# Optimization experiments

Hardware: AMD Instinct MI355X
Metric: run time of the kernel (lower is better)

Reference implementation:

```python
import jax, jax.numpy as jnp
import numpy as np

B, C, H, W = 16, 256, 96, 96


def setup_inputs() -> dict:
    key = jax.random.key(0)
    ks = jax.random.split(key, 10)
    s = 1.0 / np.sqrt(C)
    return {
        "x": jax.random.normal(ks[0], (B, C, H, W), dtype=jnp.float32) * 0.1,
        "w_theta": jax.random.normal(ks[1], (C, C), dtype=jnp.float32) * s,
        "b_theta": jax.random.normal(ks[2], (C,), dtype=jnp.float32) * 0.01,
        "w_phi": jax.random.normal(ks[3], (C, C), dtype=jnp.float32) * s,
        "b_phi": jax.random.normal(ks[4], (C,), dtype=jnp.float32) * 0.01,
        "w_g": jax.random.normal(ks[5], (C, C), dtype=jnp.float32) * s,
        "b_g": jax.random.normal(ks[6], (C,), dtype=jnp.float32) * 0.01,
        "beta_w": jax.random.normal(ks[7], (), dtype=jnp.float32) * 0.1,
        "beta_h": jax.random.normal(ks[8], (), dtype=jnp.float32) * 0.1,
        "beta_c": jax.random.normal(ks[9], (), dtype=jnp.float32) * 0.1,
    }


def _conv1x1(x, w, b):
    # 1x1 conv == channel mixing: [B,C,H,W] x [O,C] -> [B,O,H,W]
    return jnp.einsum('bchw,oc->bohw', x, w) + b[None, :, None, None]


def _axis_att(q, k, v, perm):
    # perm maps [B,C,H,W] -> [B, axis, rest...]; attention over `axis`
    qp = jnp.transpose(q, perm)
    kp = jnp.transpose(k, perm)
    vp = jnp.transpose(v, perm)
    shp = vp.shape
    n = shp[1]
    qf = qp.reshape(shp[0], n, -1)
    kf = kp.reshape(shp[0], n, -1)
    vf = vp.reshape(shp[0], n, -1)
    att = jax.nn.softmax(jnp.einsum('bik,bjk->bij', qf, kf), axis=-1)  # [B,n,n]
    out = jnp.einsum('bij,bjk->bik', att, vf).reshape(shp)
    inv = np.argsort(perm)
    return jnp.transpose(out, inv)


def reference(x, w_theta, b_theta, w_phi, b_phi, w_g, b_g, beta_w, beta_h, beta_c):
    # width: perm (0,3,2,1); height: (0,2,1,3); channel: (0,1,2,3)
    perms = [(0, 3, 2, 1), (0, 2, 1, 3), (0, 1, 2, 3)]
    betas = [beta_w, beta_h, beta_c]
    for perm, beta in zip(perms, betas):
        theta_x = _conv1x1(x, w_theta, b_theta)
        phi_x = _conv1x1(x, w_phi, b_phi)
        g_x = _conv1x1(x, w_g, b_g)
        x_t = _axis_att(theta_x, phi_x, g_x, perm)
        x = x + x_t * beta
    return x
```

## Files before the change

kernel.cpp:

```cpp
#include <hip/hip_runtime.h>
#include <hip/hip_bf16.h>

using bf16 = __hip_bfloat16;
using short8 = __attribute__((ext_vector_type(8))) short;
using float4v = __attribute__((ext_vector_type(4))) float;

#define BM 64
#define BN 64
#define BK 32
#define LDSP 40

__device__ inline short f2b(float x) {
  bf16 h = __float2bfloat16(x);
  return __builtin_bit_cast(short, h);
}

template<int F32>
__device__ inline short8 ld8e(const void* base, long eoff) {
  short8 r;
  if constexpr (F32) {
    const float* f = (const float*)base + eoff;
    #pragma unroll
    for (int i = 0; i < 8; ++i) r[i] = f2b(f[i]);
  } else {
    r = *(const short8*)((const short*)base + eoff);
  }
  return r;
}

template<int AF, int BF, int EPI, int AF32, int BF32>
__global__ __launch_bounds__(256) void gemm_k(
    const void* __restrict__ Ag, const void* __restrict__ Bg,
    void* __restrict__ Cv, void* __restrict__ Cv2, const float* __restrict__ bias,
    const float* __restrict__ betaP, const float* __restrict__ resid,
    int M, int N, int K, int lda, int ldb, int ldc,
    long sA, long sB, long sC, int ksplit, int abdiv, int msplit, int swapxy)
{
  __shared__ __align__(16) short smem[(BM + BN) * LDSP];
  short (*As)[LDSP] = (short (*)[LDSP])smem;
  short (*Bs)[LDSP] = (short (*)[LDSP])(smem + BM * LDSP);
  const int t = threadIdx.x;
  const int lane = t & 63;
  const int wave = t >> 6;
  const int wm = (wave >> 1) * 32;
  const int wn = (wave & 1) * 32;
  const int fr = lane & 15;
  const int fq = lane >> 4;
  const int bz = blockIdx.z;
  const int batch = bz / ksplit;
  const int kc = bz - batch * ksplit;
  const int Kc = K / ksplit;
  const int k0 = kc * Kc;
  int bxi = blockIdx.x, byi = blockIdx.y;
  if (swapxy) { int tmp = bxi; bxi = byi; byi = tmp; }
  const int tm0 = byi * BM;
  const int tn0 = bxi * BN;
  const long abase = (long)(batch / abdiv) * sA;
  const long bbase = (long)batch * sB;

  float4v acc[2][2] = {};

  for (int kk = 0; kk < Kc; kk += BK) {
    const int kbase = k0 + kk;
    if constexpr (AF == 0 || AF == 2) {
      int m = t >> 2;
      int kloc = (t & 3) * 8;
      int gk = kbase + kloc;
      short8 v = {};
      if (tm0 + m < M) {
        long off;
        if constexpr (AF == 0) off = abase + (long)(tm0 + m) * lda + gk;
        else                   off = abase + (long)(gk / 96) * 9216 + (long)(tm0 + m) * 96 + (gk % 96);
        v = ld8e<AF32>(Ag, off);
      }
      *(short8*)&As[m][kloc] = v;
    } else {
      int m = t & 63;
      int kg = (t >> 6) * 8;
      short8 v = {};
      if (tm0 + m < M) {
        #pragma unroll
        for (int j = 0; j < 8; ++j) {
          long off = abase + (long)(kbase + kg + j) * lda + tm0 + m;
          v[j] = AF32 ? f2b(((const float*)Ag)[off]) : ((const short*)Ag)[off];
        }
      }
      *(short8*)&As[m][kg] = v;
    }
    if constexpr (BF == 0 || BF == 2) {
      int n = t >> 2;
      int kloc = (t & 3) * 8;
      int gk = kbase + kloc;
      short8 v = {};
      if (tn0 + n < N) {
        long off;
        if constexpr (BF == 0) off = bbase + (long)(tn0 + n) * ldb + gk;
        else                   off = bbase + (long)(gk / 96) * 9216 + (long)(tn0 + n) * 96 + (gk % 96);
        v = ld8e<BF32>(Bg, off);
      }
      *(short8*)&Bs[n][kloc] = v;
    } else {
      int n = t & 63;
      int kg = (t >> 6) * 8;
      short8 v = {};
      if (tn0 + n < N) {
        #pragma unroll
        for (int j = 0; j < 8; ++j) {
          long off = bbase + (long)(kbase + kg + j) * ldb + tn0 + n;
          v[j] = BF32 ? f2b(((const float*)Bg)[off]) : ((const short*)Bg)[off];
        }
      }
      *(short8*)&Bs[n][kg] = v;
    }
    __syncthreads();
    short8 af[2], bfv[2];
    #pragma unroll
    for (int i = 0; i < 2; ++i) af[i] = *(const short8*)&As[wm + i * 16 + fr][fq * 8];
    #pragma unroll
    for (int j = 0; j < 2; ++j) bfv[j] = *(const short8*)&Bs[wn + j * 16 + fr][fq * 8];
    #pragma unroll
    for (int i = 0; i < 2; ++i)
      #pragma unroll
      for (int j = 0; j < 2; ++j)
        acc[i][j] = __builtin_amdgcn_mfma_f32_16x16x32_bf16(af[i], bfv[j], acc[i][j], 0, 0, 0);
    __syncthreads();
  }

  float beta = 0.0f;
  if constexpr (EPI >= 2) beta = *betaP;
  const long cb = (long)batch * sC;

  if constexpr (EPI == 1) {
    short* Cb = (short*)Cv;
    int rbase = tm0;
    if (Cv2 != nullptr && tm0 >= msplit) { Cb = (short*)Cv2; rbase = tm0 - msplit; }
    short (*Ct)[72] = (short (*)[72])smem;
    #pragma unroll
    for (int i = 0; i < 2; ++i)
      #pragma unroll
      for (int j = 0; j < 2; ++j)
        #pragma unroll
        for (int r = 0; r < 4; ++r) {
          int row = wm + i * 16 + fq * 4 + r;
          int col = wn + j * 16 + fr;
          float v = acc[i][j][r];
          if (bias) v += bias[tm0 + row];
          Ct[row][col] = f2b(v);
        }
    __syncthreads();
    const bool full = (tm0 + BM <= M) && (tn0 + BN <= N);
    #pragma unroll
    for (int rr = 0; rr < 2; ++rr) {
      int row = rr * 32 + (t >> 3);
      int c8 = (t & 7) * 8;
      if (full) {
        *(short8*)(Cb + cb + (long)(rbase + row) * ldc + tn0 + c8) = *(const short8*)&Ct[row][c8];
      } else if (tm0 + row < M) {
        #pragma unroll
        for (int e = 0; e < 8; ++e)
          if (tn0 + c8 + e < N)
            Cb[cb + (long)(rbase + row) * ldc + tn0 + c8 + e] = Ct[row][c8 + e];
      }
    }
  } else {
    #pragma unroll
    for (int i = 0; i < 2; ++i) {
      #pragma unroll
      for (int j = 0; j < 2; ++j) {
        #pragma unroll
        for (int r = 0; r < 4; ++r) {
          int row = tm0 + wm + i * 16 + fq * 4 + r;
          int col = tn0 + wn + j * 16 + fr;
          if (row < M && col < N) {
            float v = acc[i][j][r];
            if constexpr (EPI == 0) {
              atomicAdd((float*)Cv + cb + (long)row * ldc + col, v);
            } else if constexpr (EPI == 4) {
              float* xp = (float*)Cv;
              xp[cb + (long)row * ldc + col] += beta * v;
            } else {
              float* xp = (float*)Cv;
              long idx = cb + (long)row * ldc + col;
              xp[idx] = resid[idx] + beta * v;
            }
          }
        }
      }
    }
  }
}

__global__ __launch_bounds__(256) void softmax_k(
    const float* __restrict__ in, short* __restrict__ out, int n, int rows,
    const float* __restrict__ addj, const float* __restrict__ rowv,
    const float* __restrict__ colv)
{
  int wave = threadIdx.x >> 6;
  int lane = threadIdx.x & 63;
  int row = blockIdx.x * 4 + wave;
  if (row >= rows) return;
  int b = row / n;
  const float* r = in + (long)row * n;
  float rv = rowv ? rowv[row] : 0.0f;
  float vals[4];
  float m = -1e30f;
  #pragma unroll
  for (int i = 0; i < 4; ++i) {
    int c = lane + i * 64;
    float v = -1e30f;
    if (c < n) {
      v = r[c];
      if (addj) v += addj[(long)b * n + c];
      if (colv) v += rv * colv[c];
    }
    vals[i] = v;
    m = fmaxf(m, v);
  }
  #pragma unroll
  for (int off = 32; off > 0; off >>= 1) m = fmaxf(m, __shfl_xor(m, off));
  float s = 0.0f;
  #pragma unroll
  for (int i = 0; i < 4; ++i) {
    int c = lane + i * 64;
    float e = (c < n) ? __expf(vals[i] - m) : 0.0f;
    vals[i] = e;
    s += e;
  }
  #pragma unroll
  for (int off = 32; off > 0; off >>= 1) s += __shfl_xor(s, off);
  float inv = 1.0f / s;
  #pragma unroll
  for (int i = 0; i < 4; ++i) {
    int c = lane + i * 64;
    if (c < n) out[(long)row * n + c] = f2b(vals[i] * inv);
  }
}

__global__ __launch_bounds__(256) void sum_rows_k(
    const short* __restrict__ src, float* __restrict__ dst, int rowlen, int nrows)
{
  int wave = threadIdx.x >> 6;
  int lane = threadIdx.x & 63;
  int row = blockIdx.x * 4 + wave;
  if (row >= nrows) return;
  const short* p = src + (long)row * rowlen;
  float s = 0.0f;
  for (int k = lane; k < rowlen; k += 64)
    s += __bfloat162float(__builtin_bit_cast(bf16, p[k]));
  #pragma unroll
  for (int off = 32; off > 0; off >>= 1) s += __shfl_xor(s, off);
  if (lane == 0) dst[row] = s;
}

__global__ __launch_bounds__(256) void wv_k(
    const float* __restrict__ wphi, const float* __restrict__ btheta, float* __restrict__ wv)
{
  int c = threadIdx.x;
  float s = 0.0f;
  for (int o = 0; o < 256; ++o) s += btheta[o] * wphi[o * 256 + c];
  wv[c] = s;
}

__global__ __launch_bounds__(256) void vfull_k(
    const float* __restrict__ x, const float* __restrict__ wv, float* __restrict__ vf)
{
  long idx = (long)blockIdx.x * 256 + threadIdx.x;
  int b = (int)(idx / 9216);
  int hw = (int)(idx % 9216);
  const float* p = x + (long)b * 2359296 + hw;
  float s = 0.0f;
  for (int c = 0; c < 256; ++c) s += wv[c] * p[(long)c * 9216];
  vf[idx] = s;
}

__global__ __launch_bounds__(256) void rsum_k(
    const float* __restrict__ vf, float* __restrict__ r, int axis)
{
  int idx = blockIdx.x * 256 + threadIdx.x;
  int b = idx / 96;
  int j = idx % 96;
  const float* p = vf + (long)b * 9216;
  float s = 0.0f;
  if (axis == 0) { for (int h = 0; h < 96; ++h) s += p[h * 96 + j]; }
  else           { for (int w = 0; w < 96; ++w) s += p[j * 96 + w]; }
  r[idx] = s;
}

__global__ __launch_bounds__(256) void fill_k(
    const float* __restrict__ wth, const float* __restrict__ wg,
    const float* __restrict__ bth, const float* __restrict__ bg,
    short* __restrict__ st1, short* __restrict__ st2,
    float* __restrict__ b1, float* __restrict__ b2)
{
  int r = blockIdx.x, c = threadIdx.x;
  if (r < 256) {
    st2[r * 256 + c] = f2b(wth[r * 256 + c]);
  } else {
    short v = f2b(wg[(r - 256) * 256 + c]);
    st1[r * 256 + c] = v;
    st2[r * 256 + c] = v;
  }
  if (r == 0) { b1[c] = 0.0f; b2[c] = bth[c]; }
  if (r == 1) { b1[256 + c] = bg[c]; b2[256 + c] = bg[c]; }
}

extern "C" void kernel_launch(void* const* d_in, const int* in_sizes, int n_in,
                              void* d_out, int out_size, void* d_ws, size_t ws_size,
                              hipStream_t stream)
{
  const long TS = 37748736L;
  const long BS = 2359296L;

  float* x = (float*)d_out;
  const float* xin = (const float*)d_in[0];
  const float* wth = (const float*)d_in[1];
  const float* bth = (const float*)d_in[2];
  const float* wph = (const float*)d_in[3];
  const float* bph = (const float*)d_in[4];
  const float* wg  = (const float*)d_in[5];
  const float* bg  = (const float*)d_in[6];
  const float* beta_w = (const float*)d_in[7];
  const float* beta_h = (const float*)d_in[8];
  const float* beta_c = (const float*)d_in[9];

  const size_t need_fused = (size_t)4 * TS + 12u * 1024 * 1024;
  const bool fused = ws_size >= need_fused;

  short* bigY = (short*)d_ws;
  short* bigG = fused ? bigY + TS : bigY;
  char*  pool = (char*)(bigG + TS);
  float* attf  = (float*)pool;
  short* attb  = (short*)(attf + 1048576);
  float* Zf    = (float*)(attb + 1048576);
  short* st1   = (short*)(Zf + 1048576);
  short* st2   = st1 + 131072;
  float* bias1 = (float*)(st2 + 131072);
  float* bias2 = bias1 + 512;
  float* vfull = bias2 + 512;
  float* rbuf  = vfull + 147456;
  float* wv    = rbuf + 1536;
  float* tbar  = wv + 256;

  dim3 blk(256);

  gemm_k<1,1,1,1,1><<<dim3(4,4,1), blk, 0, stream>>>(wth, wph, st1, nullptr, nullptr, nullptr, nullptr,
      256, 256, 256, 256, 256, 256, 0, 0, 0, 1, 1, 0, 0);
  fill_k<<<512, blk, 0, stream>>>(wth, wg, bth, bg, st1, st2, bias1, bias2);
  wv_k<<<1, blk, 0, stream>>>(wph, bth, wv);

  for (int pass = 0; pass < 2; ++pass) {
    const float* xs = (pass == 0) ? xin : (const float*)x;
    if (fused) {
      gemm_k<0,1,1,0,1><<<dim3(144,8,16), blk, 0, stream>>>(st1, xs, bigY, bigG, bias1, nullptr, nullptr,
          512, 9216, 256, 256, 9216, 9216, 0, BS, BS, 1, 1, 256, 0);
    } else {
      gemm_k<0,1,1,0,1><<<dim3(144,4,16), blk, 0, stream>>>(st1, xs, bigY, nullptr, nullptr, nullptr, nullptr,
          256, 9216, 256, 256, 9216, 9216, 0, BS, BS, 1, 1, 0, 0);
    }
    vfull_k<<<576, blk, 0, stream>>>(xs, wv, vfull);
    rsum_k<<<6, blk, 0, stream>>>(vfull, rbuf, pass);
    hipMemsetAsync(attf, 0, (size_t)16 * 9216 * sizeof(float), stream);
    if (pass == 0)
      gemm_k<1,1,0,1,0><<<dim3(2,2,256), blk, 0, stream>>>(xs, bigY, attf, nullptr, nullptr, nullptr, nullptr,
          96, 96, 24576, 96, 96, 96, BS, BS, 9216, 16, 1, 0, 0);
    else
      gemm_k<2,2,0,1,0><<<dim3(2,2,256), blk, 0, stream>>>(xs, bigY, attf, nullptr, nullptr, nullptr, nullptr,
          96, 96, 24576, 0, 0, 96, BS, BS, 9216, 16, 1, 0, 0);
    softmax_k<<<384, blk, 0, stream>>>(attf, attb, 96, 1536, rbuf, nullptr, nullptr);
    if (!fused) {
      gemm_k<0,1,1,0,1><<<dim3(144,4,16), blk, 0, stream>>>(st1 + 65536, xs, bigG, nullptr, bias1 + 256,
          nullptr, nullptr, 256, 9216, 256, 256, 9216, 9216, 0, BS, BS, 1, 1, 0, 0);
    }
    if (pass == 0)
      gemm_k<0,0,5,0,0><<<dim3(2,384,16), blk, 0, stream>>>(bigG, attb, x, nullptr, nullptr, beta_w, xin,
          24576, 96, 96, 96, 96, 96, BS, 9216, BS, 1, 1, 0, 0);
    else
      gemm_k<0,1,4,0,0><<<dim3(2,2,4096), blk, 0, stream>>>(attb, bigG, x, nullptr, nullptr, beta_h, nullptr,
          96, 96, 96, 96, 96, 96, 9216, 9216, 9216, 1, 256, 0, 0);
  }

  if (fused) {
    gemm_k<0,1,1,0,1><<<dim3(144,8,16), blk, 0, stream>>>(st2, x, bigY, bigG, bias2, nullptr, nullptr,
        512, 9216, 256, 256, 9216, 9216, 0, BS, BS, 1, 1, 256, 0);
  } else {
    gemm_k<0,1,1,0,1><<<dim3(144,4,16), blk, 0, stream>>>(st2, x, bigY, nullptr, bias2, nullptr, nullptr,
        256, 9216, 256, 256, 9216, 9216, 0, BS, BS, 1, 1, 0, 0);
  }
  hipMemsetAsync(Zf, 0, (size_t)16 * 256 * 256 * sizeof(float), stream);
  gemm_k<0,0,0,0,1><<<dim3(4,4,64), blk, 0, stream>>>(bigY, x, Zf, nullptr, nullptr, nullptr, nullptr,
      256, 256, 9216, 9216, 9216, 256, BS, BS, 65536, 4, 1, 0, 0);
  sum_rows_k<<<1024, blk, 0, stream>>>(bigY, tbar, 9216, 4096);
  hipMemsetAsync(attf, 0, (size_t)16 * 256 * 256 * sizeof(float), stream);
  gemm_k<0,0,0,1,1><<<dim3(4,4,16), blk, 0, stream>>>(Zf, wph, attf, nullptr, nullptr, nullptr, nullptr,
      256, 256, 256, 256, 256, 256, 65536, 0, 65536, 1, 1, 0, 0);
  softmax_k<<<1024, blk, 0, stream>>>(attf, attb, 256, 4096, nullptr, tbar, bph);
  if (!fused) {
    gemm_k<0,1,1,0,1><<<dim3(144,4,16), blk, 0, stream>>>(st1 + 65536, x, bigG, nullptr, bias1 + 256,
        nullptr, nullptr, 256, 9216, 256, 256, 9216, 9216, 0, BS, BS, 1, 1, 0, 0);
  }
  gemm_k<0,1,4,0,0><<<dim3(144,4,16), blk, 0, stream>>>(attb, bigG, x, nullptr, nullptr, beta_c, nullptr,
      256, 9216, 256, 256, 9216, 9216, 65536, BS, BS, 1, 1, 0, 0);
}
```

Measured before the change: 1.432 ms.

## Keep a bf16 shadow copy of x and XOR-swizzle LDS tiles

Adds a bf16 copy of the activation x, produced once by a conversion kernel and then refreshed inside the residual-update epilogues. GEMMs that read x can then load bf16 instead of fp32 and convert per element, which halves their input traffic. The LDS tile column offsets are also XOR-swizzled by row to cut bank conflicts on MFMA fragment reads. The cost is an extra workspace buffer, a larger threshold before the full path is used, and an extra bf16 store in the epilogue.

```diff
diff --git a/kernel.cpp b/kernel.cpp
--- a/kernel.cpp
+++ b/kernel.cpp
@@ -14,6 +14,8 @@
   bf16 h = __float2bfloat16(x);
   return __builtin_bit_cast(short, h);
 }
+
+__device__ inline int swz(int row, int g) { return (g ^ ((row >> 3) & 3)) * 8; }
 
 template<int F32>
 __device__ inline short8 ld8e(const void* base, long eoff) {
@@ -33,6 +35,7 @@
     const void* __restrict__ Ag, const void* __restrict__ Bg,
     void* __restrict__ Cv, void* __restrict__ Cv2, const float* __restrict__ bias,
     const float* __restrict__ betaP, const float* __restrict__ resid,
+    short* __restrict__ xbout,
     int M, int N, int K, int lda, int ldb, int ldc,
     long sA, long sB, long sC, int ksplit, int abdiv, int msplit, int swapxy)
 {
@@ -73,19 +76,19 @@
         else                   off = abase + (long)(gk / 96) * 9216 + (long)(tm0 + m) * 96 + (gk % 96);
         v = ld8e<AF32>(Ag, off);
       }
-      *(short8*)&As[m][kloc] = v;
+      *(short8*)&As[m][swz(m, t & 3)] = v;
     } else {
       int m = t & 63;
-      int kg = (t >> 6) * 8;
+      int kg = t >> 6;
       short8 v = {};
       if (tm0 + m < M) {
         #pragma unroll
         for (int j = 0; j < 8; ++j) {
-          long off = abase + (long)(kbase + kg + j) * lda + tm0 + m;
+          long off = abase + (long)(kbase + kg * 8 + j) * lda + tm0 + m;
           v[j] = AF32 ? f2b(((const float*)Ag)[off]) : ((const short*)Ag)[off];
         }
       }
-      *(short8*)&As[m][kg] = v;
+      *(short8*)&As[m][swz(m, kg)] = v;
     }
     if constexpr (BF == 0 || BF == 2) {
       int n = t >> 2;
@@ -98,26 +101,26 @@
         else                   off = bbase + (long)(gk / 96) * 9216 + (long)(tn0 + n) * 96 + (gk % 96);
         v = ld8e<BF32>(Bg, off);
       }
-      *(short8*)&Bs[n][kloc] = v;
+      *(short8*)&Bs[n][swz(n, t & 3)] = v;
     } else {
       int n = t & 63;
-      int kg = (t >> 6) * 8;
+      int kg = t >> 6;
       short8 v = {};
       if (tn0 + n < N) {
         #pragma unroll
         for (int j = 0; j < 8; ++j) {
-          long off = bbase + (long)(kbase + kg + j) * ldb + tn0 + n;
+          long off = bbase + (long)(kbase + kg * 8 + j) * ldb + tn0 + n;
           v[j] = BF32 ? f2b(((const float*)Bg)[off]) : ((const short*)Bg)[off];
         }
       }
-      *(short8*)&Bs[n][kg] = v;
+      *(short8*)&Bs[n][swz(n, kg)] = v;
     }
     __syncthreads();
     short8 af[2], bfv[2];
     #pragma unroll
-    for (int i = 0; i < 2; ++i) af[i] = *(const short8*)&As[wm + i * 16 + fr][fq * 8];
-    #pragma unroll
-    for (int j = 0; j < 2; ++j) bfv[j] = *(const short8*)&Bs[wn + j * 16 + fr][fq * 8];
+    for (int i = 0; i < 2; ++i) { int r = wm + i * 16 + fr; af[i] = *(const short8*)&As[r][swz(r, fq)]; }
+    #pragma unroll
+    for (int j = 0; j < 2; ++j) { int r = wn + j * 16 + fr; bfv[j] = *(const short8*)&Bs[r][swz(r, fq)]; }
     #pragma unroll
     for (int i = 0; i < 2; ++i)
       #pragma unroll
@@ -177,17 +180,35 @@
               atomicAdd((float*)Cv + cb + (long)row * ldc + col, v);
             } else if constexpr (EPI == 4) {
               float* xp = (float*)Cv;
-              xp[cb + (long)row * ldc + col] += beta * v;
+              long idx = cb + (long)row * ldc + col;
+              float nv = xp[idx] + beta * v;
+              xp[idx] = nv;
+              if (xbout) xbout[idx] = f2b(nv);
             } else {
               float* xp = (float*)Cv;
               long idx = cb + (long)row * ldc + col;
-              xp[idx] = resid[idx] + beta * v;
+              float nv = resid[idx] + beta * v;
+              xp[idx] = nv;
+              if (xbout) xbout[idx] = f2b(nv);
             }
           }
         }
       }
     }
   }
+}
+
+__global__ __launch_bounds__(256) void cvt_k(
+    const float* __restrict__ in, short* __restrict__ out, long n)
+{
+  long i = ((long)blockIdx.x * 256 + threadIdx.x) * 8;
+  if (i >= n) return;
+  const float4v* p = (const float4v*)(in + i);
+  float4v a = p[0], b = p[1];
+  short8 v;
+  v[0] = f2b(a[0]); v[1] = f2b(a[1]); v[2] = f2b(a[2]); v[3] = f2b(a[3]);
+  v[4] = f2b(b[0]); v[5] = f2b(b[1]); v[6] = f2b(b[2]); v[7] = f2b(b[3]);
+  *(short8*)(out + i) = v;
 }
 
 __global__ __launch_bounds__(256) void softmax_k(
@@ -310,6 +331,7 @@
 {
   const long TS = 37748736L;
   const long BS = 2359296L;
+  const size_t POOL = 12u * 1024 * 1024;
 
   float* x = (float*)d_out;
   const float* xin = (const float*)d_in[0];
@@ -323,12 +345,13 @@
   const float* beta_h = (const float*)d_in[8];
   const float* beta_c = (const float*)d_in[9];
 
-  const size_t need_fused = (size_t)4 * TS + 12u * 1024 * 1024;
-  const bool fused = ws_size >= need_fused;
-
-  short* bigY = (short*)d_ws;
-  short* bigG = fused ? bigY + TS : bigY;
-  char*  pool = (char*)(bigG + TS);
+  const size_t need_full = (size_t)6 * TS + POOL;
+  const bool full = ws_size >= need_full;
+
+  short* xb   = (short*)d_ws;
+  short* bigY = xb + TS;
+  char*  pool = (char*)(bigY + TS);
+  short* bigG = full ? (short*)(pool + POOL) : bigY;
   float* attf  = (float*)pool;
   short* attb  = (short*)(attf + 1048576);
   float* Zf    = (float*)(attb + 1048576);
@@ -344,60 +367,61 @@
   dim3 blk(256);
 
   gemm_k<1,1,1,1,1><<<dim3(4,4,1), blk, 0, stream>>>(wth, wph, st1, nullptr, nullptr, nullptr, nullptr,
-      256, 256, 256, 256, 256, 256, 0, 0, 0, 1, 1, 0, 0);
+      nullptr, 256, 256, 256, 256, 256, 256, 0, 0, 0, 1, 1, 0, 0);
   fill_k<<<512, blk, 0, stream>>>(wth, wg, bth, bg, st1, st2, bias1, bias2);
   wv_k<<<1, blk, 0, stream>>>(wph, bth, wv);
+  cvt_k<<<18432, blk, 0, stream>>>(xin, xb, TS);
 
   for (int pass = 0; pass < 2; ++pass) {
     const float* xs = (pass == 0) ? xin : (const float*)x;
-    if (fused) {
-      gemm_k<0,1,1,0,1><<<dim3(144,8,16), blk, 0, stream>>>(st1, xs, bigY, bigG, bias1, nullptr, nullptr,
-          512, 9216, 256, 256, 9216, 9216, 0, BS, BS, 1, 1, 256, 0);
+    if (full) {
+      gemm_k<0,1,1,0,0><<<dim3(144,8,16), blk, 0, stream>>>(st1, xb, bigY, bigG, bias1, nullptr, nullptr,
+          nullptr, 512, 9216, 256, 256, 9216, 9216, 0, BS, BS, 1, 1, 256, 0);
     } else {
-      gemm_k<0,1,1,0,1><<<dim3(144,4,16), blk, 0, stream>>>(st1, xs, bigY, nullptr, nullptr, nullptr, nullptr,
-          256, 9216, 256, 256, 9216, 9216, 0, BS, BS, 1, 1, 0, 0);
+      gemm_k<0,1,1,0,0><<<dim3(144,4,16), blk, 0, stream>>>(st1, xb, bigY, nullptr, nullptr, nullptr, nullptr,
+          nullptr, 256, 9216, 256, 256, 9216, 9216, 0, BS, BS, 1, 1, 0, 0);
     }
     vfull_k<<<576, blk, 0, stream>>>(xs, wv, vfull);
     rsum_k<<<6, blk, 0, stream>>>(vfull, rbuf, pass);
     hipMemsetAsync(attf, 0, (size_t)16 * 9216 * sizeof(float), stream);
     if (pass == 0)
-      gemm_k<1,1,0,1,0><<<dim3(2,2,256), blk, 0, stream>>>(xs, bigY, attf, nullptr, nullptr, nullptr, nullptr,
-          96, 96, 24576, 96, 96, 96, BS, BS, 9216, 16, 1, 0, 0);
+      gemm_k<1,1,0,0,0><<<dim3(2,2,256), blk, 0, stream>>>(xb, bigY, attf, nullptr, nullptr, nullptr, nullptr,
+          nullptr, 96, 96, 24576, 96, 96, 96, BS, BS, 9216, 16, 1, 0, 0);
     else
-      gemm_k<2,2,0,1,0><<<dim3(2,2,256), blk, 0, stream>>>(xs, bigY, attf, nullptr, nullptr, nullptr, nullptr,
-          96, 96, 24576, 0, 0, 96, BS, BS, 9216, 16, 1, 0, 0);
+      gemm_k<2,2,0,0,0><<<dim3(2,2,256), blk, 0, stream>>>(xb, bigY, attf, nullptr, nullptr, nullptr, nullptr,
+          nullptr, 96, 96, 24576, 0, 0, 96, BS, BS, 9216, 16, 1, 0, 0);
     softmax_k<<<384, blk, 0, stream>>>(attf, attb, 96, 1536, rbuf, nullptr, nullptr);
-    if (!fused) {
-      gemm_k<0,1,1,0,1><<<dim3(144,4,16), blk, 0, stream>>>(st1 + 65536, xs, bigG, nullptr, bias1 + 256,
-          nullptr, nullptr, 256, 9216, 256, 256, 9216, 9216, 0, BS, BS, 1, 1, 0, 0);
+    if (!full) {
+      gemm_k<0,1,1,0,0><<<dim3(144,4,16), blk, 0, stream>>>(st1 + 65536, xb, bigG, nullptr, bias1 + 256,
+          nullptr, nullptr, nullptr, 256, 9216, 256, 256, 9216, 9216, 0, BS, BS, 1, 1, 0, 0);
     }
     if (pass == 0)
       gemm_k<0,0,5,0,0><<<dim3(2,384,16), blk, 0, stream>>>(bigG, attb, x, nullptr, nullptr, beta_w, xin,
-          24576, 96, 96, 96, 96, 96, BS, 9216, BS, 1, 1, 0, 0);
+          xb, 24576, 96, 96, 96, 96, 96, BS, 9216, BS, 1, 1, 0, 0);
     else
       gemm_k<0,1,4,0,0><<<dim3(2,2,4096), blk, 0, stream>>>(attb, bigG, x, nullptr, nullptr, beta_h, nullptr,
-          96, 96, 96, 96, 96, 96, 9216, 9216, 9216, 1, 256, 0, 0);
-  }
-
-  if (fused) {
-    gemm_k<0,1,1,0,1><<<dim3(144,8,16), blk, 0, stream>>>(st2, x, bigY, bigG, bias2, nullptr, nullptr,
-        512, 9216, 256, 256, 9216, 9216, 0, BS, BS, 1, 1, 256, 0);
+          xb, 96, 96, 96, 96, 96, 96, 9216, 9216, 9216, 1, 256, 0, 0);
+  }
+
+  if (full) {
+    gemm_k<0,1,1,0,0><<<dim3(144,8,16), blk, 0, stream>>>(st2, xb, bigY, bigG, bias2, nullptr, nullptr,
+        nullptr, 512, 9216, 256, 256, 9216, 9216, 0, BS, BS, 1, 1, 256, 0);
   } else {
-    gemm_k<0,1,1,0,1><<<dim3(144,4,16), blk, 0, stream>>>(st2, x, bigY, nullptr, bias2, nullptr, nullptr,
-        256, 9216, 256, 256, 9216, 9216, 0, BS, BS, 1, 1, 0, 0);
+    gemm_k<0,1,1,0,0><<<dim3(144,4,16), blk, 0, stream>>>(st2, xb, bigY, nullptr, bias2, nullptr, nullptr,
+        nullptr, 256, 9216, 256, 256, 9216, 9216, 0, BS, BS, 1, 1, 0, 0);
   }
   hipMemsetAsync(Zf, 0, (size_t)16 * 256 * 256 * sizeof(float), stream);
-  gemm_k<0,0,0,0,1><<<dim3(4,4,64), blk, 0, stream>>>(bigY, x, Zf, nullptr, nullptr, nullptr, nullptr,
-      256, 256, 9216, 9216, 9216, 256, BS, BS, 65536, 4, 1, 0, 0);
+  gemm_k<0,0,0,0,0><<<dim3(4,4,64), blk, 0, stream>>>(bigY, xb, Zf, nullptr, nullptr, nullptr, nullptr,
+      nullptr, 256, 256, 9216, 9216, 9216, 256, BS, BS, 65536, 4, 1, 0, 0);
   sum_rows_k<<<1024, blk, 0, stream>>>(bigY, tbar, 9216, 4096);
   hipMemsetAsync(attf, 0, (size_t)16 * 256 * 256 * sizeof(float), stream);
   gemm_k<0,0,0,1,1><<<dim3(4,4,16), blk, 0, stream>>>(Zf, wph, attf, nullptr, nullptr, nullptr, nullptr,
-      256, 256, 256, 256, 256, 256, 65536, 0, 65536, 1, 1, 0, 0);
+      nullptr, 256, 256, 256, 256, 256, 256, 65536, 0, 65536, 1, 1, 0, 0);
   softmax_k<<<1024, blk, 0, stream>>>(attf, attb, 256, 4096, nullptr, tbar, bph);
-  if (!fused) {
-    gemm_k<0,1,1,0,1><<<dim3(144,4,16), blk, 0, stream>>>(st1 + 65536, x, bigG, nullptr, bias1 + 256,
-        nullptr, nullptr, 256, 9216, 256, 256, 9216, 9216, 0, BS, BS, 1, 1, 0, 0);
+  if (!full) {
+    gemm_k<0,1,1,0,0><<<dim3(144,4,16), blk, 0, stream>>>(st1 + 65536, xb, bigG, nullptr, bias1 + 256,
+        nullptr, nullptr, nullptr, 256, 9216, 256, 256, 9216, 9216, 0, BS, BS, 1, 1, 0, 0);
   }
   gemm_k<0,1,4,0,0><<<dim3(144,4,16), blk, 0, stream>>>(attb, bigG, x, nullptr, nullptr, beta_c, nullptr,
-      256, 9216, 256, 256, 9216, 9216, 65536, BS, BS, 1, 1, 0, 0);
-}
+      nullptr, 256, 9216, 256, 256, 9216, 9216, 65536, BS, BS, 1, 1, 0, 0);
+}
```

Result: slower. 1.560 ms (+8.9%).
